# Optimization experiments

Hardware: AMD Instinct MI355X
Metric: run time of the kernel (lower is better)

Reference implementation:

```python
import jax, jax.numpy as jnp
import numpy as np

N = 6144   # number of patches (bag size)
L = 1024   # input feature dim
D = 512    # GCN hidden dim
ALPHA = 0.4
THRESH = 0.5


def _layernorm(x, g, b):
    m = jnp.mean(x, axis=-1, keepdims=True)
    v = jnp.mean((x - m) ** 2, axis=-1, keepdims=True)
    return (x - m) / jnp.sqrt(v + 1e-5) * g + b


def _l1rows(x):
    # F.normalize(x, p=1): row-wise L1 normalize with eps=1e-12
    return x / jnp.maximum(jnp.sum(jnp.abs(x), axis=1, keepdims=True), 1e-12)


def _nonlin(x, w1, b1, g, bn, w2, b2):
    h = jax.nn.relu(_layernorm(x @ w1 + b1, g, bn))
    return h @ w2 + b2


def _gcn(x, adj, w, b, g, bn):
    # GraphConvolution: adj @ (x @ W) + bias, then LayerNorm + ReLU
    return jax.nn.relu(_layernorm(adj @ (x @ w) + b, g, bn))


def setup_inputs() -> dict:
    key = jax.random.key(0)
    ks = iter(jax.random.split(key, 64))

    def nrm(shape, s=0.02):
        return jax.random.normal(next(ks), shape, jnp.float32) * s

    inp = {
        'x_path': jax.random.normal(next(ks), (N, L), jnp.float32),
        'maps': jax.random.uniform(next(ks), (N, N), jnp.float32) * 0.1,
    }
    for pre in ['nl0', 'nl1']:
        inp[pre + '_w1'] = nrm((L, D)); inp[pre + '_b1'] = jnp.zeros((D,), jnp.float32)
        inp[pre + '_g'] = jnp.ones((D,), jnp.float32); inp[pre + '_bn'] = jnp.zeros((D,), jnp.float32)
        inp[pre + '_w2'] = nrm((D, D)); inp[pre + '_b2'] = jnp.zeros((D,), jnp.float32)
    for pre in ['gc0', 'gc1', 'gc2', 'ga0', 'ga1', 'ga2']:
        inp[pre + '_w'] = nrm((D, D)); inp[pre + '_b'] = jnp.zeros((D,), jnp.float32)
        inp[pre + '_g'] = jnp.ones((D,), jnp.float32); inp[pre + '_bn'] = jnp.zeros((D,), jnp.float32)
    inp['attn_wa'] = nrm((L, 256)); inp['attn_ba'] = jnp.zeros((256,), jnp.float32)
    inp['attn_wb'] = nrm((L, 256)); inp['attn_bb'] = jnp.zeros((256,), jnp.float32)
    inp['attn_wc'] = nrm((256, 1)); inp['attn_bc'] = jnp.zeros((1,), jnp.float32)
    inp['cls_w'] = nrm((L, 4), 0.001)
    inp['ln_g'] = jnp.ones((L,), jnp.float32); inp['ln_b'] = jnp.zeros((L,), jnp.float32)
    return inp


def reference(x_path, maps,
              nl0_w1, nl0_b1, nl0_g, nl0_bn, nl0_w2, nl0_b2,
              nl1_w1, nl1_b1, nl1_g, nl1_bn, nl1_w2, nl1_b2,
              gc0_w, gc0_b, gc0_g, gc0_bn,
              gc1_w, gc1_b, gc1_g, gc1_bn,
              gc2_w, gc2_b, gc2_g, gc2_bn,
              ga0_w, ga0_b, ga0_g, ga0_bn,
              ga1_w, ga1_b, ga1_g, ga1_bn,
              ga2_w, ga2_b, ga2_g, ga2_bn,
              attn_wa, attn_ba, attn_wb, attn_bb, attn_wc, attn_bc,
              cls_w, ln_g, ln_b):
    # cosine-similarity adjacency: L2-normalize rows, gram matrix, min-max, threshold
    xn = x_path / jnp.maximum(jnp.linalg.norm(x_path, axis=1, keepdims=True), 1e-12)
    cs = xn @ xn.T                                       # [N,N]
    cs = (cs - cs.min()) / (cs.max() - cs.min())
    cs = (cs >= THRESH).astype(jnp.float32)

    # gated attention (eval mode, no dropout): A = Wc (tanh(Wa x) * sigmoid(Wb x))
    a = jnp.tanh(x_path @ attn_wa + attn_ba)
    bg = jax.nn.sigmoid(x_path @ attn_wb + attn_bb)
    agg = (a * bg) @ attn_wc + attn_bc                   # [N,1]

    s = jax.nn.sigmoid(agg)
    aw = s * s.T                                         # outer product [N,N]
    aw = (aw - aw.min()) / (aw.max() - aw.min())
    aw = ALPHA + (1.0 - ALPHA) * aw + maps

    cs = _l1rows(cs)
    aw = _l1rows(aw)

    x0 = _nonlin(x_path, nl0_w1, nl0_b1, nl0_g, nl0_bn, nl0_w2, nl0_b2)
    x1 = _nonlin(x_path, nl1_w1, nl1_b1, nl1_g, nl1_bn, nl1_w2, nl1_b2)

    g1 = _gcn(x0, cs, gc0_w, gc0_b, gc0_g, gc0_bn)
    g1 = _gcn(g1, cs, gc1_w, gc1_b, gc1_g, gc1_bn)
    g1 = _gcn(g1, cs, gc2_w, gc2_b, gc2_g, gc2_bn)

    g2 = _gcn(x1, aw, ga0_w, ga0_b, ga0_g, ga0_bn)
    g2 = _gcn(g2, aw, ga1_w, ga1_b, ga1_g, ga1_bn)
    g2 = _gcn(g2, aw, ga2_w, ga2_b, ga2_g, ga2_bn)

    gcf = jnp.concatenate([g2, g1], axis=1)              # [N, 1024]

    n = x_path.shape[0]
    trans = (cs @ agg) / (n ** 0.5)                      # [N,1]
    fw = jax.nn.softmax(0.3 * trans + 0.7 * agg, axis=0) # softmax over patches
    pooled = fw.T @ gcf                                  # [1, 1024]
    pooled = _layernorm(pooled, ln_g, ln_b)

    logits = pooled @ cls_w                              # [1, 4]
    y_hat = jnp.argmax(logits, axis=1, keepdims=True)    # topk k=1 index
    hazards = jax.nn.sigmoid(logits)
    surv = jnp.cumprod(1.0 - hazards, axis=1)
    return hazards, surv, y_hat
```

## Files before the change

kernel.cpp:

```cpp
#include <hip/hip_runtime.h>

#define N_ 6144
#define L_ 1024
#define D_ 512
#define H_ 256
#define SPARSE_MAX 64u

typedef unsigned short u16;
typedef unsigned long long u64;
typedef __attribute__((ext_vector_type(4))) float f32x4;
typedef __attribute__((ext_vector_type(8))) short s16x8;
typedef __attribute__((ext_vector_type(4))) short s16x4;

__device__ __forceinline__ u16 f2b(float f){
  unsigned u = __float_as_uint(f);
  u += 0x7FFFu + ((u >> 16) & 1u);
  return (u16)(u >> 16);
}
__device__ __forceinline__ float b2f(u16 h){ return __uint_as_float(((unsigned)h) << 16); }
__device__ __forceinline__ unsigned fkey(float f){
  unsigned u = __float_as_uint(f);
  return (u & 0x80000000u) ? ~u : (u | 0x80000000u);
}
__device__ __forceinline__ float funkey(unsigned k){
  unsigned u = (k & 0x80000000u) ? (k & 0x7FFFFFFFu) : ~k;
  return __uint_as_float(u);
}
__device__ __forceinline__ float wave_sum(float v){
  #pragma unroll
  for(int o=32;o;o>>=1) v += __shfl_xor(v,o);
  return v;
}
__device__ __forceinline__ float wave_max(float v){
  #pragma unroll
  for(int o=32;o;o>>=1) v = fmaxf(v,__shfl_xor(v,o));
  return v;
}
__device__ __forceinline__ float wave_min(float v){
  #pragma unroll
  for(int o=32;o;o>>=1) v = fminf(v,__shfl_xor(v,o));
  return v;
}
__device__ __forceinline__ float blk_sum256(float v){
  __shared__ float sm[4];
  v = wave_sum(v);
  __syncthreads();
  if((threadIdx.x&63)==0) sm[threadIdx.x>>6]=v;
  __syncthreads();
  return sm[0]+sm[1]+sm[2]+sm[3];
}
__device__ __forceinline__ float blk_min256(float v){
  __shared__ float sm[4];
  v = wave_min(v);
  __syncthreads();
  if((threadIdx.x&63)==0) sm[threadIdx.x>>6]=v;
  __syncthreads();
  return fminf(fminf(sm[0],sm[1]),fminf(sm[2],sm[3]));
}
__device__ __forceinline__ float blk_max256(float v){
  __shared__ float sm[4];
  v = wave_max(v);
  __syncthreads();
  if((threadIdx.x&63)==0) sm[threadIdx.x>>6]=v;
  __syncthreads();
  return fmaxf(fmaxf(sm[0],sm[1]),fmaxf(sm[2],sm[3]));
}

template<int VW> __device__ __forceinline__ void waitv(){
  if constexpr(VW==8) asm volatile("s_waitcnt vmcnt(8)" ::: "memory");
  else if constexpr(VW==4) asm volatile("s_waitcnt vmcnt(4)" ::: "memory");
  else asm volatile("s_waitcnt vmcnt(0)" ::: "memory");
}

#define STG4(bb,k0) do{ \
  __builtin_amdgcn_global_load_lds((__attribute__((address_space(1))) void*)(gA0+(k0)), (__attribute__((address_space(3))) void*)(lds + (bb)*4096 + (wid<<9)),        16, 0, 0); \
  __builtin_amdgcn_global_load_lds((__attribute__((address_space(1))) void*)(gA1+(k0)), (__attribute__((address_space(3))) void*)(lds + (bb)*4096 + 2048 + (wid<<9)), 16, 0, 0); \
  __builtin_amdgcn_global_load_lds((__attribute__((address_space(1))) void*)(gB0+(k0)), (__attribute__((address_space(3))) void*)(lds + 12288 + (bb)*4096 + (wid<<9)),        16, 0, 0); \
  __builtin_amdgcn_global_load_lds((__attribute__((address_space(1))) void*)(gB1+(k0)), (__attribute__((address_space(3))) void*)(lds + 12288 + (bb)*4096 + 2048 + (wid<<9)), 16, 0, 0); \
}while(0)

template<int MODE>
__global__ __launch_bounds__(256) void gemm_bt(
  const u16* __restrict__ A, const u16* __restrict__ Bt,
  int M, int Nc, int K,
  u16* __restrict__ Cb, unsigned* __restrict__ mmx,
  const unsigned* __restrict__ gate)
{
  if (gate && gate[2] <= SPARSE_MAX) return;
  __shared__ __align__(16) u16 lds[3*4096*2];
  const int tid = threadIdx.x;
  const int wid = tid>>6, lane = tid&63;

  int m0, n0;
  if (MODE==1){
    int t = (int)blockIdx.x;
    t = (t&7)*147 + (t>>3);
    int i=0, rem=t;
    while (rem >= 48-i){ rem -= 48-i; ++i; }
    m0 = i<<7; n0 = (i+rem)<<7;
  } else {
    const int gx = gridDim.x;
    int lid = blockIdx.y*gx + blockIdx.x;
    const int nwg = gx*gridDim.y;
    if ((nwg & 7) == 0) {
      const int chunk = nwg >> 3;
      lid = (lid & 7)*chunk + (lid >> 3);
    }
    m0 = (lid/gx)<<7; n0 = (lid%gx)<<7;
  }
  const int wr = wid>>1, wc = wid&1;

  const int Klen = K / gridDim.z;
  const int kbeg = blockIdx.z * Klen;

  const int srow = (wid<<4) + (lane>>2);
  const int scol = (lane&3)<<3;
  const u16* gA0 = A  + (size_t)(m0+srow   )*K + scol;
  const u16* gA1 = A  + (size_t)(m0+srow+64)*K + scol;
  const u16* gB0 = Bt + (size_t)(n0+srow   )*K + scol;
  const u16* gB1 = Bt + (size_t)(n0+srow+64)*K + scol;

  f32x4 acc[4][4] = {};
  const int lr = lane&15, lk = (lane>>4)<<3;

  const int NIT = Klen>>5;
  STG4(0, kbeg);
  STG4(1, kbeg+32);
  STG4(2, kbeg+64);

  for (int it=0; it<NIT-2; ++it){
    const int b = it - (it/3)*3;
    waitv<8>();
    __builtin_amdgcn_s_barrier();
    const u16* baseA = lds + b*4096;
    const u16* baseB = lds + 12288 + b*4096;
    s16x8 af[4], bfr[4];
    #pragma unroll
    for(int m=0;m<4;m++) af[m]  = *(const s16x8*)(baseA + ((wr<<6)+(m<<4)+lr)*32 + lk);
    #pragma unroll
    for(int n=0;n<4;n++) bfr[n] = *(const s16x8*)(baseB + ((wc<<6)+(n<<4)+lr)*32 + lk);
    asm volatile("s_waitcnt lgkmcnt(0)" ::: "memory");
    __builtin_amdgcn_sched_barrier(0);
    __builtin_amdgcn_s_barrier();
    if (it+3 < NIT) STG4(b, kbeg + ((it+3)<<5));
    #pragma unroll
    for(int m=0;m<4;m++)
      #pragma unroll
      for(int n=0;n<4;n++)
        acc[m][n] = __builtin_amdgcn_mfma_f32_16x16x32_bf16(af[m], bfr[n], acc[m][n], 0,0,0);
  }
  {
    const int it = NIT-2; const int b = it - (it/3)*3;
    waitv<4>();
    __builtin_amdgcn_s_barrier();
    const u16* baseA = lds + b*4096;
    const u16* baseB = lds + 12288 + b*4096;
    s16x8 af[4], bfr[4];
    #pragma unroll
    for(int m=0;m<4;m++) af[m]  = *(const s16x8*)(baseA + ((wr<<6)+(m<<4)+lr)*32 + lk);
    #pragma unroll
    for(int n=0;n<4;n++) bfr[n] = *(const s16x8*)(baseB + ((wc<<6)+(n<<4)+lr)*32 + lk);
    #pragma unroll
    for(int m=0;m<4;m++)
      #pragma unroll
      for(int n=0;n<4;n++)
        acc[m][n] = __builtin_amdgcn_mfma_f32_16x16x32_bf16(af[m], bfr[n], acc[m][n], 0,0,0);
  }
  {
    const int it = NIT-1; const int b = it - (it/3)*3;
    waitv<0>();
    __builtin_amdgcn_s_barrier();
    const u16* baseA = lds + b*4096;
    const u16* baseB = lds + 12288 + b*4096;
    s16x8 af[4], bfr[4];
    #pragma unroll
    for(int m=0;m<4;m++) af[m]  = *(const s16x8*)(baseA + ((wr<<6)+(m<<4)+lr)*32 + lk);
    #pragma unroll
    for(int n=0;n<4;n++) bfr[n] = *(const s16x8*)(baseB + ((wc<<6)+(n<<4)+lr)*32 + lk);
    #pragma unroll
    for(int m=0;m<4;m++)
      #pragma unroll
      for(int n=0;n<4;n++)
        acc[m][n] = __builtin_amdgcn_mfma_f32_16x16x32_bf16(af[m], bfr[n], acc[m][n], 0,0,0);
  }

  float tmin = 3.0e38f, tmax = -3.0e38f;
  if (MODE==1){
    #pragma unroll
    for(int m=0;m<4;m++)
      #pragma unroll
      for(int n=0;n<4;n++){
        f32x4 v = acc[m][n];
        #pragma unroll
        for(int e=0;e<4;e++){ tmin = fminf(tmin,v[e]); tmax = fmaxf(tmax,v[e]); }
      }
  }

  __syncthreads();
  u16* lC = lds;
  {
    const int rb_l = (wr<<6) + ((lane>>4)<<2);
    const int cb_l = (wc<<6) + lr;
    #pragma unroll
    for(int m=0;m<4;m++)
      #pragma unroll
      for(int n=0;n<4;n++){
        f32x4 v = acc[m][n];
        #pragma unroll
        for(int e=0;e<4;e++)
          lC[(rb_l+(m<<4)+e)*128 + cb_l+(n<<4)] = f2b(v[e]);
      }
  }
  __syncthreads();
  u16* Cp = (MODE==0) ? (Cb + (size_t)blockIdx.z * M * Nc) : Cb;
  #pragma unroll
  for(int q=0;q<8;q++){
    int c = (q<<8) + tid;
    int r = c>>4, cc = (c&15)<<3;
    s16x8 v = *(const s16x8*)(lC + r*128 + cc);
    if (MODE==1)
      __builtin_nontemporal_store(v, (s16x8*)(Cp + (size_t)(m0+r)*Nc + n0 + cc));
    else
      *(s16x8*)(Cp + (size_t)(m0+r)*Nc + n0 + cc) = v;
  }

  if (MODE==1){
    tmin = wave_min(tmin); tmax = wave_max(tmax);
    __shared__ float rmn[4], rmx[4];
    if(lane==0){ rmn[wid]=tmin; rmx[wid]=tmax; }
    __syncthreads();
    if(tid==0){
      float mn=fminf(fminf(rmn[0],rmn[1]),fminf(rmn[2],rmn[3]));
      float mx=fmaxf(fmaxf(rmx[0],rmx[1]),fmaxf(rmx[2],rmx[3]));
      atomicMin(mmx+0, fkey(mn));
      atomicMax(mmx+1, fkey(mx));
    }
  }
}

__global__ __launch_bounds__(256) void mirror_lower(u16* __restrict__ C)
{
  int c0 = blockIdx.x<<5, r0 = blockIdx.y<<5;
  if ((r0>>7) >= (c0>>7)) return;
  __shared__ u16 t[32][33];
  int tx = threadIdx.x&31, ty = threadIdx.x>>5;
  #pragma unroll
  for(int i=0;i<32;i+=8) t[ty+i][tx] = C[(size_t)(r0+ty+i)*N_ + c0+tx];
  __syncthreads();
  #pragma unroll
  for(int i=0;i<32;i+=8)
    __builtin_nontemporal_store(t[tx][ty+i], C + (size_t)(c0+ty+i)*N_ + r0+tx);
}

struct TDesc { const float* src; u16* dst; int R; int C; int base; };
struct TDescs { TDesc d[12]; };
__global__ __launch_bounds__(256) void transpose_cast_multi(TDescs ds, int nd)
{
  int b = (int)blockIdx.x;
  int k = 0;
  for (int q=1;q<nd;q++) if (b >= ds.d[q].base) k = q;
  const float* src = ds.d[k].src;
  u16* dst = ds.d[k].dst;
  int R = ds.d[k].R, C = ds.d[k].C;
  int lt = b - ds.d[k].base;
  int tc = C>>5;
  int bx = lt % tc, by = lt / tc;
  __shared__ float t[32][33];
  int c0 = bx<<5, r0 = by<<5;
  int tx = threadIdx.x&31, ty = threadIdx.x>>5;
  #pragma unroll
  for(int i=0;i<32;i+=8) t[ty+i][tx] = src[(size_t)(r0+ty+i)*C + c0+tx];
  __syncthreads();
  #pragma unroll
  for(int i=0;i<32;i+=8) dst[(size_t)(c0+ty+i)*R + r0+tx] = f2b(t[tx][ty+i]);
}

__global__ __launch_bounds__(256) void transpose_sum_bf(
  const u16* __restrict__ src, size_t pstr, int nsp,
  u16* __restrict__ dst, int R, int C, const unsigned* __restrict__ gate)
{
  if (gate && gate[2] <= SPARSE_MAX) return;
  __shared__ float t[32][33];
  int c0 = blockIdx.x<<5, r0 = blockIdx.y<<5;
  int tx = threadIdx.x&31, ty = threadIdx.x>>5;
  #pragma unroll
  for(int i=0;i<32;i+=8){
    float v = 0;
    for(int p=0;p<nsp;p++)
      v += b2f(src[(size_t)p*pstr + (size_t)(r0+ty+i)*C + c0+tx]);
    t[ty+i][tx] = v;
  }
  __syncthreads();
  #pragma unroll
  for(int i=0;i<32;i+=8) dst[(size_t)(c0+ty+i)*R + r0+tx] = f2b(t[tx][ty+i]);
}

__global__ __launch_bounds__(256) void prep_x(const float* __restrict__ x,
  u16* __restrict__ xb, u16* __restrict__ xnb)
{
  int row = blockIdx.x, t = threadIdx.x;
  const float* p = x + (size_t)row*L_ + (t<<2);
  f32x4 v = *(const f32x4*)p;
  float ss = v[0]*v[0]+v[1]*v[1]+v[2]*v[2]+v[3]*v[3];
  float tot = blk_sum256(ss);
  float inv = 1.0f/fmaxf(sqrtf(tot), 1e-12f);
  u16* pb = xb  + (size_t)row*L_ + (t<<2);
  u16* pn = xnb + (size_t)row*L_ + (t<<2);
  #pragma unroll
  for(int k=0;k<4;k++){ pb[k]=f2b(v[k]); pn[k]=f2b(v[k]*inv); }
}

__global__ __launch_bounds__(256) void attn_epi(const u16* __restrict__ SPA,
  size_t pstr, int nsp,
  const float* __restrict__ ba, const float* __restrict__ bb,
  const float* __restrict__ wc, const float* __restrict__ bc,
  float* __restrict__ agg, float* __restrict__ s)
{
  int row = (blockIdx.x<<2) + (threadIdx.x>>6);
  int lane = threadIdx.x&63;
  float a[4]={0,0,0,0}, b[4]={0,0,0,0};
  for(int p=0;p<nsp;p++){
    s16x4 ua = *(const s16x4*)(SPA + (size_t)p*pstr + (size_t)row*1536 + (lane<<2));
    s16x4 ub = *(const s16x4*)(SPA + (size_t)p*pstr + (size_t)row*1536 + 256 + (lane<<2));
    #pragma unroll
    for(int j=0;j<4;j++){ a[j]+=b2f((u16)ua[j]); b[j]+=b2f((u16)ub[j]); }
  }
  float acc=0;
  #pragma unroll
  for(int j=0;j<4;j++){
    int h = (lane<<2)+j;
    float tv = tanhf(a[j]+ba[h]);
    float sg = 1.0f/(1.0f+expf(-(b[j]+bb[h])));
    acc += tv*sg*wc[h];
  }
  acc = wave_sum(acc);
  if(lane==0){
    float v = acc + bc[0];
    agg[row]=v;
    s[row]=1.0f/(1.0f+expf(-v));
  }
}

__global__ __launch_bounds__(256) void s_stats(const float* __restrict__ s, float* __restrict__ sc){
  int t=threadIdx.x;
  float mn=3e38f, mx=-3e38f;
  for(int i=t;i<N_;i+=256){ float v=s[i]; mn=fminf(mn,v); mx=fmaxf(mx,v); }
  float MN=blk_min256(mn);
  float MX=blk_max256(mx);
  if(t==0){ sc[0]=MN; sc[1]=MX; }
}

__global__ __launch_bounds__(256) void aw_write(const float* __restrict__ maps, const float* __restrict__ s,
  const float* __restrict__ sc, u16* __restrict__ awb)
{
  int i = blockIdx.x, t = threadIdx.x;
  float smin = sc[0], smax = sc[1];
  float mn = smin*smin, mx = smax*smax;
  float beta = 0.6f/(mx-mn);
  float c1 = 0.4f - beta*mn;
  float si = s[i];
  const float* mrow = maps + (size_t)i*N_;
  float mv[24];
  float part = 0;
  #pragma unroll
  for(int q=0;q<24;q++){
    int j = t + (q<<8);
    mv[q] = c1 + beta*si*s[j] + mrow[j];
    part += mv[q];
  }
  float r = blk_sum256(part);
  float inv = 1.0f/fmaxf(r, 1e-12f);
  u16* orow = awb + (size_t)i*N_;
  #pragma unroll
  for(int q=0;q<24;q++)
    __builtin_nontemporal_store(f2b(mv[q]*inv), orow + t + (q<<8));
}

__global__ __launch_bounds__(256) void ln_epi512(const u16* __restrict__ Y, size_t pstr, int nsp,
  int rs, int cbase,
  const float* __restrict__ ki,
  const float* __restrict__ bias, const float* __restrict__ g, const float* __restrict__ bn,
  u16* __restrict__ outb,
  const unsigned* __restrict__ gate)
{
  if (gate && gate[2] <= SPARSE_MAX) return;
  int row = (blockIdx.x<<2)+(threadIdx.x>>6);
  int lane = threadIdx.x&63;
  int c0 = lane<<3;
  float v[8] = {0,0,0,0,0,0,0,0};
  for(int p=0;p<nsp;p++){
    s16x8 u = *(const s16x8*)(Y + (size_t)p*pstr + (size_t)row*rs + cbase + c0);
    #pragma unroll
    for(int j=0;j<8;j++) v[j] += b2f((u16)u[j]);
  }
  float scale = ki ? (1.0f/ki[row]) : 1.0f;
  float sum=0, ssum=0;
  #pragma unroll
  for(int j=0;j<8;j++){ v[j] = v[j]*scale + bias[c0+j]; sum+=v[j]; ssum+=v[j]*v[j]; }
  sum = wave_sum(sum); ssum = wave_sum(ssum);
  float m = sum*(1.0f/D_);
  float var = ssum*(1.0f/D_) - m*m;
  float invsd = rsqrtf(var + 1e-5f);
  u16 ob[8];
  #pragma unroll
  for(int j=0;j<8;j++){
    float o = (v[j]-m)*invsd*g[c0+j] + bn[c0+j];
    o = fmaxf(o, 0.0f);
    ob[j] = f2b(o);
  }
  *(s16x8*)(outb + (size_t)row*D_ + c0) = *(s16x8*)ob;
}

__global__ __launch_bounds__(256) void bias_cast(const u16* __restrict__ Y, size_t pstr, int nsp,
  const float* __restrict__ b, u16* __restrict__ outb)
{
  size_t idx = ((size_t)blockIdx.x*256 + threadIdx.x)<<3;
  float v[8] = {0,0,0,0,0,0,0,0};
  for(int p=0;p<nsp;p++){
    s16x8 u = *(const s16x8*)(Y + (size_t)p*pstr + idx);
    #pragma unroll
    for(int j=0;j<8;j++) v[j] += b2f((u16)u[j]);
  }
  int c = (int)(idx & (D_-1));
  u16 ob[8];
  #pragma unroll
  for(int k=0;k<8;k++) ob[k] = f2b(v[k]+b[c+k]);
  *(s16x8*)(outb+idx) = *(s16x8*)ob;
}

__global__ void init_k(unsigned* mmx){
  mmx[0]=0xFFFFFFFFu; mmx[1]=0u; mmx[2]=0u;
}

__global__ __launch_bounds__(256) void binarize(const u16* __restrict__ csb,
  unsigned* __restrict__ mmx, const float* __restrict__ agg,
  float* __restrict__ ki, float* __restrict__ z, u64* __restrict__ bm)
{
  int i = blockIdx.x, t = threadIdx.x;
  int lane = t&63, w = t>>6;
  float mn = funkey(mmx[0]), mx = funkey(mmx[1]);
  float th = mn + 0.5f*(mx-mn);
  const u16* row = csb + (size_t)i*N_;
  u64* bmrow = bm + (size_t)i*96;
  float cnt = 0, dot = 0;
  #pragma unroll
  for(int q=0;q<24;q++){
    int j = t + (q<<8);
    bool on = b2f(row[j]) >= th;
    u64 mask = __ballot(on);
    if(lane==0) bmrow[(q<<2)+w] = mask;
    if(on){ cnt += 1.0f; dot += agg[j]; }
  }
  float k = blk_sum256(cnt);
  float dt = blk_sum256(dot);
  if(t==0){
    ki[i] = k;
    float tr = dt/(k*sqrtf((float)N_));
    z[i] = 0.3f*tr + 0.7f*agg[i];
    if (k > (float)SPARSE_MAX)
      atomicMax(mmx+2, (unsigned)(k+0.5f));
  }
}

__global__ __launch_bounds__(256) void binarize_store(u16* __restrict__ csb,
  const unsigned* __restrict__ mmx)
{
  if (mmx[2] <= SPARSE_MAX) return;
  int i = blockIdx.x, t = threadIdx.x;
  float mn = funkey(mmx[0]), mx = funkey(mmx[1]);
  float th = mn + 0.5f*(mx-mn);
  u16* row = csb + (size_t)i*N_;
  #pragma unroll
  for(int q=0;q<24;q++){
    int j = t + (q<<8);
    row[j] = (b2f(row[j]) >= th) ? (u16)0x3F80 : (u16)0;
  }
}

__global__ __launch_bounds__(256) void gather_ln(const u64* __restrict__ bm,
  const u16* __restrict__ SPp, size_t pstr, int nsp,
  const unsigned* __restrict__ gate, const float* __restrict__ ki,
  const float* __restrict__ bias, const float* __restrict__ g, const float* __restrict__ bn,
  u16* __restrict__ outb)
{
  if (gate[2] > SPARSE_MAX) return;
  int i = blockIdx.x, t = threadIdx.x;
  __shared__ u64 wbuf[96];
  __shared__ u16 idx[SPARSE_MAX];
  __shared__ int nn_s;
  if (t < 96) wbuf[t] = bm[(size_t)i*96 + t];
  __syncthreads();
  if (t == 0){
    int nn = 0;
    for(int k=0;k<96;k++){
      u64 m = wbuf[k];
      while(m && nn < (int)SPARSE_MAX){
        int b = __ffsll((long long)m) - 1;
        m &= m - 1;
        idx[nn++] = (u16)((k<<6) + b);
      }
    }
    nn_s = nn;
  }
  __syncthreads();
  int nn = nn_s;
  float a0=0, a1=0;
  for(int k=0;k<nn;k++){
    size_t jb = (size_t)idx[k]*512;
    for(int p=0;p<nsp;p++){
      a0 += b2f(SPp[p*pstr + jb + t]);
      a1 += b2f(SPp[p*pstr + jb + t + 256]);
    }
  }
  float scale = 1.0f/ki[i];
  float v0 = a0*scale + bias[t];
  float v1 = a1*scale + bias[t+256];
  float sum  = blk_sum256(v0+v1);
  float ssum = blk_sum256(v0*v0+v1*v1);
  float m = sum*(1.0f/512.0f);
  float var = ssum*(1.0f/512.0f) - m*m;
  float inv = rsqrtf(var+1e-5f);
  float o0 = fmaxf((v0-m)*inv*g[t]+bn[t], 0.0f);
  float o1 = fmaxf((v1-m)*inv*g[t+256]+bn[t+256], 0.0f);
  outb[(size_t)i*512 + t]       = f2b(o0);
  outb[(size_t)i*512 + t + 256] = f2b(o1);
}

__global__ __launch_bounds__(1024) void softmax_prep(const float* __restrict__ z,
  float* __restrict__ e, float* __restrict__ sexp)
{
  int t = threadIdx.x;
  __shared__ float sm[16];
  float mx=-3e38f;
  for(int i=t;i<N_;i+=1024) mx=fmaxf(mx,z[i]);
  mx = wave_max(mx);
  if((t&63)==0) sm[t>>6]=mx;
  __syncthreads();
  float zm = sm[0];
  #pragma unroll
  for(int w=1;w<16;w++) zm=fmaxf(zm,sm[w]);
  __syncthreads();
  float sum=0;
  for(int i=t;i<N_;i+=1024){ float ee=expf(z[i]-zm); e[i]=ee; sum+=ee; }
  sum = wave_sum(sum);
  if((t&63)==0) sm[t>>6]=sum;
  __syncthreads();
  if(t==0){ float S=0; for(int w=0;w<16;w++) S+=sm[w]; *sexp=S; }
}

__global__ __launch_bounds__(256) void pooled_partial(const float* __restrict__ e,
  const u16* __restrict__ g2b, const u16* __restrict__ g1b, float* __restrict__ part)
{
  int b = blockIdx.x, t = threadIdx.x;
  float a0=0,a1=0,a2=0,a3=0;
  for(int r=0;r<192;r++){
    int row = b*192+r;
    float w = e[row];
    a0 += w * b2f(g2b[(size_t)row*D_ + t]);
    a1 += w * b2f(g2b[(size_t)row*D_ + t+256]);
    a2 += w * b2f(g1b[(size_t)row*D_ + t]);
    a3 += w * b2f(g1b[(size_t)row*D_ + t+256]);
  }
  part[(size_t)b*1024 + t]      = a0;
  part[(size_t)b*1024 + t+256]  = a1;
  part[(size_t)b*1024 + t+512]  = a2;
  part[(size_t)b*1024 + t+768]  = a3;
}

__global__ __launch_bounds__(1024) void final_k(const float* __restrict__ part, const float* __restrict__ sexp,
  const float* __restrict__ lng, const float* __restrict__ lnb,
  const float* __restrict__ clsw, float* __restrict__ out)
{
  int t = threadIdx.x;
  __shared__ float red[16];
  __shared__ float smv[1024];
  __shared__ float lgs[4];
  float p=0;
  for(int b=0;b<32;b++) p += part[b*1024 + t];
  p /= sexp[0];
  float w = wave_sum(p);
  if((t&63)==0) red[t>>6]=w;
  __syncthreads();
  float tot=0;
  #pragma unroll
  for(int i2=0;i2<16;i2++) tot+=red[i2];
  float m = tot*(1.0f/1024.0f);
  __syncthreads();
  float d = p-m;
  w = wave_sum(d*d);
  if((t&63)==0) red[t>>6]=w;
  __syncthreads();
  tot=0;
  #pragma unroll
  for(int i2=0;i2<16;i2++) tot+=red[i2];
  float var = tot*(1.0f/1024.0f);
  float y = d*rsqrtf(var+1e-5f)*lng[t] + lnb[t];
  smv[t]=y;
  __syncthreads();
  if(t<4){
    float lg=0;
    for(int j=0;j<1024;j++) lg += smv[j]*clsw[j*4+t];
    lgs[t]=lg;
  }
  __syncthreads();
  if(t==0){
    float h[4];
    int am=0; float best=lgs[0];
    #pragma unroll
    for(int c2=0;c2<4;c2++){ h[c2]=1.0f/(1.0f+expf(-lgs[c2])); if(lgs[c2]>best){best=lgs[c2];am=c2;} }
    float sv=1.0f;
    #pragma unroll
    for(int c2=0;c2<4;c2++){ out[c2]=h[c2]; sv*=(1.0f-h[c2]); out[4+c2]=sv; }
    out[8]=(float)am;
  }
}

extern "C" void kernel_launch(void* const* d_in, const int* in_sizes, int n_in,
                              void* d_out, int out_size, void* d_ws, size_t ws_size,
                              hipStream_t stream)
{
  const float* x_path =(const float*)d_in[0];
  const float* maps   =(const float*)d_in[1];
  const float* nl0_w1 =(const float*)d_in[2];
  const float* nl0_b1 =(const float*)d_in[3];
  const float* nl0_g  =(const float*)d_in[4];
  const float* nl0_bn =(const float*)d_in[5];
  const float* nl0_w2 =(const float*)d_in[6];
  const float* nl0_b2 =(const float*)d_in[7];
  const float* nl1_w1 =(const float*)d_in[8];
  const float* nl1_b1 =(const float*)d_in[9];
  const float* nl1_g  =(const float*)d_in[10];
  const float* nl1_bn =(const float*)d_in[11];
  const float* nl1_w2 =(const float*)d_in[12];
  const float* nl1_b2 =(const float*)d_in[13];
  const float *gw[6], *gb[6], *gg[6], *gbn[6];
  for(int l=0;l<6;l++){
    gw[l]  = (const float*)d_in[14+l*4+0];
    gb[l]  = (const float*)d_in[14+l*4+1];
    gg[l]  = (const float*)d_in[14+l*4+2];
    gbn[l] = (const float*)d_in[14+l*4+3];
  }
  const float* attn_wa=(const float*)d_in[38];
  const float* attn_ba=(const float*)d_in[39];
  const float* attn_wb=(const float*)d_in[40];
  const float* attn_bb=(const float*)d_in[41];
  const float* attn_wc=(const float*)d_in[42];
  const float* attn_bc=(const float*)d_in[43];
  const float* cls_w  =(const float*)d_in[44];
  const float* ln_g   =(const float*)d_in[45];
  const float* ln_b   =(const float*)d_in[46];

  char* ws=(char*)d_ws;
  size_t off=0;
  auto alc=[&](size_t b)->char*{ char* p=ws+off; off=(off+b+255)&~(size_t)255; return p; };
  u16* BIG = (u16*)alc((size_t)N_*N_*2);
  u16* XB  = (u16*)alc((size_t)N_*L_*2);
  u16* XNB = (u16*)alc((size_t)N_*L_*2);
  u16* WT_proj=(u16*)alc((size_t)1536*L_*2);
  u16* WT_nl0w2=(u16*)alc((size_t)D_*D_*2);
  u16* WT_nl1w2=(u16*)alc((size_t)D_*D_*2);
  u16* WT_g[6];
  for(int l=0;l<6;l++) WT_g[l]=(u16*)alc((size_t)D_*D_*2);
  u16* SP = (u16*)alc((size_t)2*N_*1536*2);
  u16* XWT=(u16*)alc((size_t)D_*N_*2);
  u16* XA0=(u16*)alc((size_t)N_*D_*2);
  u16* XA1=(u16*)alc((size_t)N_*D_*2);
  u16* X0B=(u16*)alc((size_t)N_*D_*2);
  u16* X1B=(u16*)alc((size_t)N_*D_*2);
  u16* YS =(u16*)alc((size_t)N_*D_*2);
  u64* BM =(u64*)alc((size_t)N_*96*8);
  float* PART=(float*)alc((size_t)32*1024*4);
  float* AGG=(float*)alc(N_*4);
  float* SS =(float*)alc(N_*4);
  float* KI =(float*)alc(N_*4);
  float* Z  =(float*)alc(N_*4);
  float* E  =(float*)alc(N_*4);
  float* SC =(float*)alc(256);
  unsigned* MMX=(unsigned*)alc(256);
  float* SEXP=(float*)alc(256);

  const size_t PS_D = (size_t)N_*D_;
  const size_t PS_P = (size_t)N_*1536;

  init_k<<<1,1,0,stream>>>(MMX);
  prep_x<<<N_,256,0,stream>>>(x_path, XB, XNB);

  {
    TDescs ds;
    int base = 0;
    auto add=[&](int k, const float* s, u16* d, int R, int C){
      ds.d[k] = {s, d, R, C, base};
      base += (R>>5)*(C>>5);
    };
    add(0,  attn_wa, WT_proj,                   L_, H_);
    add(1,  attn_wb, WT_proj + (size_t)256*L_,  L_, H_);
    add(2,  nl0_w1,  WT_proj + (size_t)512*L_,  L_, D_);
    add(3,  nl1_w1,  WT_proj + (size_t)1024*L_, L_, D_);
    add(4,  nl0_w2,  WT_nl0w2, D_, D_);
    add(5,  nl1_w2,  WT_nl1w2, D_, D_);
    for(int l=0;l<6;l++) add(6+l, gw[l], WT_g[l], D_, D_);
    transpose_cast_multi<<<base,256,0,stream>>>(ds, 12);
  }

  gemm_bt<0><<<dim3(1536/128, N_/128, 2),256,0,stream>>>(XB, WT_proj, N_, 1536, L_, SP, nullptr, nullptr);
  attn_epi<<<N_/4,256,0,stream>>>(SP, PS_P, 2, attn_ba, attn_bb, attn_wc, attn_bc, AGG, SS);
  s_stats<<<1,256,0,stream>>>(SS,SC);
  aw_write<<<N_,256,0,stream>>>(maps,SS,SC,BIG);

  ln_epi512<<<N_/4,256,0,stream>>>(SP,PS_P,2, 1536,1024, nullptr, nl1_b1,nl1_g,nl1_bn, XA1, nullptr);
  ln_epi512<<<N_/4,256,0,stream>>>(SP,PS_P,2, 1536, 512, nullptr, nl0_b1,nl0_g,nl0_bn, XA0, nullptr);

  gemm_bt<0><<<dim3(D_/128,N_/128,4),256,0,stream>>>(XA1, WT_nl1w2, N_,D_,D_, SP, nullptr, nullptr);
  bias_cast<<<(N_*D_/8)/256,256,0,stream>>>(SP,PS_D,4, nl1_b2, X1B);

  {
    const u16* cur=X1B;
    for(int l=0;l<3;l++){
      int gi = 3+l;
      gemm_bt<0><<<dim3(D_/128,N_/128,4),256,0,stream>>>(cur, WT_g[gi], N_,D_,D_, SP, nullptr, nullptr);
      transpose_sum_bf<<<dim3(D_/32, N_/32),256,0,stream>>>(SP, PS_D, 4, XWT, N_, D_, nullptr);
      gemm_bt<0><<<dim3(D_/128,N_/128,6),256,0,stream>>>(BIG, XWT, N_,D_,N_, SP, nullptr, nullptr);
      u16* nxt = (l==0)? XA1 : (l==1)? YS : X1B;
      ln_epi512<<<N_/4,256,0,stream>>>(SP,PS_D,6, 512,0, nullptr, gb[gi],gg[gi],gbn[gi], nxt, nullptr);
      cur = nxt;
    }
  }

  gemm_bt<0><<<dim3(D_/128,N_/128,4),256,0,stream>>>(XA0, WT_nl0w2, N_,D_,D_, SP, nullptr, nullptr);
  bias_cast<<<(N_*D_/8)/256,256,0,stream>>>(SP,PS_D,4, nl0_b2, X0B);

  gemm_bt<1><<<dim3(1176,1,1),256,0,stream>>>(XNB, XNB, N_,N_,L_, BIG, MMX, nullptr);
  mirror_lower<<<dim3(N_/32, N_/32),256,0,stream>>>(BIG);
  binarize<<<N_,256,0,stream>>>(BIG, MMX, AGG, KI, Z, BM);
  binarize_store<<<N_,256,0,stream>>>(BIG, MMX);

  {
    const u16* cur=X0B;
    for(int l=0;l<3;l++){
      int gi = l;
      gemm_bt<0><<<dim3(D_/128,N_/128,4),256,0,stream>>>(cur, WT_g[gi], N_,D_,D_, SP, nullptr, nullptr);
      transpose_sum_bf<<<dim3(D_/32, N_/32),256,0,stream>>>(SP, PS_D, 4, XWT, N_, D_, MMX);
      gemm_bt<0><<<dim3(D_/128,N_/128,6),256,0,stream>>>(BIG, XWT, N_,D_,N_, SP, nullptr, MMX);
      u16* nxt = (l==0)? XA1 : (l==1)? XA0 : X0B;
      gather_ln<<<N_,256,0,stream>>>(BM, SP, PS_D, 4, MMX, KI, gb[gi],gg[gi],gbn[gi], nxt);
      ln_epi512<<<N_/4,256,0,stream>>>(SP,PS_D,6, 512,0, KI, gb[gi],gg[gi],gbn[gi], nxt, MMX);
      cur = nxt;
    }
  }

  softmax_prep<<<1,1024,0,stream>>>(Z,E,SEXP);
  pooled_partial<<<32,256,0,stream>>>(E,X1B,X0B,PART);
  final_k<<<1,1024,0,stream>>>(PART,SEXP,ln_g,ln_b,cls_w,(float*)d_out);

  (void)in_sizes;(void)n_in;(void)out_size;(void)ws_size;
}
```

Baseline: 789.3 us.

## Binarize upper triangle with symmetric atomics, gate mirror, fuse LN epilogues, raise split-K

The cosine-similarity binarization now reads only the upper triangle of the symmetric matrix. It writes the transposed bits through 64-bit atomicOr into a pre-zeroed bitmask, and a second kernel computes row counts and dot products from those bits. The mirror-lower copy now runs only when the dense path is needed, so it is skipped in the sparse case. The two projection LayerNorm epilogues are merged into one launch, and the adjacency GEMM split-K goes from 6 to 8 with an enlarged partial buffer. The cost is a memset, scattered atomics, and extra partial-sum traffic.

```diff
diff --git a/kernel.cpp b/kernel.cpp
--- a/kernel.cpp
+++ b/kernel.cpp
@@ -238,8 +238,10 @@
   }
 }
 
-__global__ __launch_bounds__(256) void mirror_lower(u16* __restrict__ C)
-{
+__global__ __launch_bounds__(256) void mirror_lower(u16* __restrict__ C,
+  const unsigned* __restrict__ gate)
+{
+  if (gate[2] <= SPARSE_MAX) return;
   int c0 = blockIdx.x<<5, r0 = blockIdx.y<<5;
   if ((r0>>7) >= (c0>>7)) return;
   __shared__ u16 t[32][33];
@@ -411,6 +413,42 @@
   *(s16x8*)(outb + (size_t)row*D_ + c0) = *(s16x8*)ob;
 }
 
+__global__ __launch_bounds__(256) void ln_epi_proj(const u16* __restrict__ Y, size_t pstr, int nsp,
+  const float* __restrict__ b1, const float* __restrict__ g1, const float* __restrict__ n1, u16* __restrict__ o1,
+  const float* __restrict__ b0, const float* __restrict__ g0, const float* __restrict__ n0, u16* __restrict__ o0)
+{
+  const int sel = blockIdx.y;
+  const int cbase = sel ? 512 : 1024;
+  const float* bias = sel ? b0 : b1;
+  const float* g    = sel ? g0 : g1;
+  const float* bn   = sel ? n0 : n1;
+  u16* outb         = sel ? o0 : o1;
+  int row = (blockIdx.x<<2)+(threadIdx.x>>6);
+  int lane = threadIdx.x&63;
+  int c0 = lane<<3;
+  float v[8] = {0,0,0,0,0,0,0,0};
+  for(int p=0;p<nsp;p++){
+    s16x8 u = *(const s16x8*)(Y + (size_t)p*pstr + (size_t)row*1536 + cbase + c0);
+    #pragma unroll
+    for(int j=0;j<8;j++) v[j] += b2f((u16)u[j]);
+  }
+  float sum=0, ssum=0;
+  #pragma unroll
+  for(int j=0;j<8;j++){ v[j] = v[j] + bias[c0+j]; sum+=v[j]; ssum+=v[j]*v[j]; }
+  sum = wave_sum(sum); ssum = wave_sum(ssum);
+  float m = sum*(1.0f/D_);
+  float var = ssum*(1.0f/D_) - m*m;
+  float invsd = rsqrtf(var + 1e-5f);
+  u16 ob[8];
+  #pragma unroll
+  for(int j=0;j<8;j++){
+    float o = (v[j]-m)*invsd*g[c0+j] + bn[c0+j];
+    o = fmaxf(o, 0.0f);
+    ob[j] = f2b(o);
+  }
+  *(s16x8*)(outb + (size_t)row*D_ + c0) = *(s16x8*)ob;
+}
+
 __global__ __launch_bounds__(256) void bias_cast(const u16* __restrict__ Y, size_t pstr, int nsp,
   const float* __restrict__ b, u16* __restrict__ outb)
 {
@@ -432,9 +470,8 @@
   mmx[0]=0xFFFFFFFFu; mmx[1]=0u; mmx[2]=0u;
 }
 
-__global__ __launch_bounds__(256) void binarize(const u16* __restrict__ csb,
-  unsigned* __restrict__ mmx, const float* __restrict__ agg,
-  float* __restrict__ ki, float* __restrict__ z, u64* __restrict__ bm)
+__global__ __launch_bounds__(256) void binarize_tri(const u16* __restrict__ csb,
+  const unsigned* __restrict__ mmx, u64* __restrict__ bm)
 {
   int i = blockIdx.x, t = threadIdx.x;
   int lane = t&63, w = t>>6;
@@ -442,18 +479,38 @@
   float th = mn + 0.5f*(mx-mn);
   const u16* row = csb + (size_t)i*N_;
   u64* bmrow = bm + (size_t)i*96;
+  const int w0 = i>>6;
+  for (int wq = w0 + w; wq < 96; wq += 4){
+    int j = (wq<<6) + lane;
+    bool on = (j >= i) && (b2f(row[j]) >= th);
+    u64 mask = __ballot(on);
+    if (lane == 0){
+      if (wq == w0) atomicOr((u64*)(bmrow+wq), mask);
+      else bmrow[wq] = mask;
+    }
+    if (on && j > i)
+      atomicOr((u64*)(bm + (size_t)j*96 + w0), 1ull << (i&63));
+  }
+}
+
+__global__ __launch_bounds__(256) void binarize_fin(const u64* __restrict__ bm,
+  unsigned* __restrict__ mmx, const float* __restrict__ agg,
+  float* __restrict__ ki, float* __restrict__ z)
+{
+  int i = blockIdx.x, t = threadIdx.x;
   float cnt = 0, dot = 0;
-  #pragma unroll
-  for(int q=0;q<24;q++){
-    int j = t + (q<<8);
-    bool on = b2f(row[j]) >= th;
-    u64 mask = __ballot(on);
-    if(lane==0) bmrow[(q<<2)+w] = mask;
-    if(on){ cnt += 1.0f; dot += agg[j]; }
-  }
-  float k = blk_sum256(cnt);
+  if (t < 96){
+    u64 m = bm[(size_t)i*96 + t];
+    cnt = (float)__popcll(m);
+    while (m){
+      int b = __ffsll((long long)m) - 1;
+      m &= m - 1;
+      dot += agg[(t<<6) + b];
+    }
+  }
+  float k  = blk_sum256(cnt);
   float dt = blk_sum256(dot);
-  if(t==0){
+  if (t==0){
     ki[i] = k;
     float tr = dt/(k*sqrtf((float)N_));
     z[i] = 0.3f*tr + 0.7f*agg[i];
@@ -661,7 +718,7 @@
   u16* WT_nl1w2=(u16*)alc((size_t)D_*D_*2);
   u16* WT_g[6];
   for(int l=0;l<6;l++) WT_g[l]=(u16*)alc((size_t)D_*D_*2);
-  u16* SP = (u16*)alc((size_t)2*N_*1536*2);
+  u16* SP = (u16*)alc((size_t)8*N_*D_*2);
   u16* XWT=(u16*)alc((size_t)D_*N_*2);
   u16* XA0=(u16*)alc((size_t)N_*D_*2);
   u16* XA1=(u16*)alc((size_t)N_*D_*2);
@@ -683,6 +740,7 @@
   const size_t PS_P = (size_t)N_*1536;
 
   init_k<<<1,1,0,stream>>>(MMX);
+  hipMemsetAsync(BM, 0, (size_t)N_*96*8, stream);
   prep_x<<<N_,256,0,stream>>>(x_path, XB, XNB);
 
   {
@@ -707,8 +765,8 @@
   s_stats<<<1,256,0,stream>>>(SS,SC);
   aw_write<<<N_,256,0,stream>>>(maps,SS,SC,BIG);
 
-  ln_epi512<<<N_/4,256,0,stream>>>(SP,PS_P,2, 1536,1024, nullptr, nl1_b1,nl1_g,nl1_bn, XA1, nullptr);
-  ln_epi512<<<N_/4,256,0,stream>>>(SP,PS_P,2, 1536, 512, nullptr, nl0_b1,nl0_g,nl0_bn, XA0, nullptr);
+  ln_epi_proj<<<dim3(N_/4,2),256,0,stream>>>(SP,PS_P,2,
+    nl1_b1,nl1_g,nl1_bn,XA1, nl0_b1,nl0_g,nl0_bn,XA0);
 
   gemm_bt<0><<<dim3(D_/128,N_/128,4),256,0,stream>>>(XA1, WT_nl1w2, N_,D_,D_, SP, nullptr, nullptr);
   bias_cast<<<(N_*D_/8)/256,256,0,stream>>>(SP,PS_D,4, nl1_b2, X1B);
@@ -719,9 +777,9 @@
       int gi = 3+l;
       gemm_bt<0><<<dim3(D_/128,N_/128,4),256,0,stream>>>(cur, WT_g[gi], N_,D_,D_, SP, nullptr, nullptr);
       transpose_sum_bf<<<dim3(D_/32, N_/32),256,0,stream>>>(SP, PS_D, 4, XWT, N_, D_, nullptr);
-      gemm_bt<0><<<dim3(D_/128,N_/128,6),256,0,stream>>>(BIG, XWT, N_,D_,N_, SP, nullptr, nullptr);
+      gemm_bt<0><<<dim3(D_/128,N_/128,8),256,0,stream>>>(BIG, XWT, N_,D_,N_, SP, nullptr, nullptr);
       u16* nxt = (l==0)? XA1 : (l==1)? YS : X1B;
-      ln_epi512<<<N_/4,256,0,stream>>>(SP,PS_D,6, 512,0, nullptr, gb[gi],gg[gi],gbn[gi], nxt, nullptr);
+      ln_epi512<<<N_/4,256,0,stream>>>(SP,PS_D,8, 512,0, nullptr, gb[gi],gg[gi],gbn[gi], nxt, nullptr);
       cur = nxt;
     }
   }
@@ -730,8 +788,9 @@
   bias_cast<<<(N_*D_/8)/256,256,0,stream>>>(SP,PS_D,4, nl0_b2, X0B);
 
   gemm_bt<1><<<dim3(1176,1,1),256,0,stream>>>(XNB, XNB, N_,N_,L_, BIG, MMX, nullptr);
-  mirror_lower<<<dim3(N_/32, N_/32),256,0,stream>>>(BIG);
-  binarize<<<N_,256,0,stream>>>(BIG, MMX, AGG, KI, Z, BM);
+  binarize_tri<<<N_,256,0,stream>>>(BIG, MMX, BM);
+  binarize_fin<<<N_,256,0,stream>>>(BM, MMX, AGG, KI, Z);
+  mirror_lower<<<dim3(N_/32, N_/32),256,0,stream>>>(BIG, MMX);
   binarize_store<<<N_,256,0,stream>>>(BIG, MMX);
 
   {
@@ -740,10 +799,10 @@
       int gi = l;
       gemm_bt<0><<<dim3(D_/128,N_/128,4),256,0,stream>>>(cur, WT_g[gi], N_,D_,D_, SP, nullptr, nullptr);
       transpose_sum_bf<<<dim3(D_/32, N_/32),256,0,stream>>>(SP, PS_D, 4, XWT, N_, D_, MMX);
-      gemm_bt<0><<<dim3(D_/128,N_/128,6),256,0,stream>>>(BIG, XWT, N_,D_,N_, SP, nullptr, MMX);
+      gemm_bt<0><<<dim3(D_/128,N_/128,8),256,0,stream>>>(BIG, XWT, N_,D_,N_, SP, nullptr, MMX);
       u16* nxt = (l==0)? XA1 : (l==1)? XA0 : X0B;
       gather_ln<<<N_,256,0,stream>>>(BM, SP, PS_D, 4, MMX, KI, gb[gi],gg[gi],gbn[gi], nxt);
-      ln_epi512<<<N_/4,256,0,stream>>>(SP,PS_D,6, 512,0, KI, gb[gi],gg[gi],gbn[gi], nxt, MMX);
+      ln_epi512<<<N_/4,256,0,stream>>>(SP,PS_D,8, 512,0, KI, gb[gi],gg[gi],gbn[gi], nxt, MMX);
       cur = nxt;
     }
   }
```

Result: faster. 768.2 us, median of 2 (-2.7%).
